# Performance work log

Measured on AMD Instinct MI355X. Metric: run time of the kernel, lower is better.

The kernel has to match this reference:

```python
import jax, jax.numpy as jnp
import numpy as np
from jax import lax

C, NORI, NROT, K, PAD = 256, 8, 2, 3, 1
B, H, W = 16, 64, 64
EPS = 1e-5


def setup_inputs() -> dict:
    key = jax.random.key(0)
    k1, k2, k3 = jax.random.split(key, 3)
    x = jax.random.normal(k1, (B, C, H, W), dtype=jnp.float32)
    # rotate_arf() output: [nRot*C, nOri*C, K, K]
    weight_all = jax.random.normal(k2, (NROT * C, NORI * C, K, K), dtype=jnp.float32) * 0.02
    bias_all = jax.random.normal(k3, (NROT * C,), dtype=jnp.float32) * 0.02
    alpha = jnp.float32(1.0)
    gamma = jnp.ones((C,), dtype=jnp.float32)
    beta = jnp.zeros((C,), dtype=jnp.float32)
    return {"x": x, "weight_all": weight_all, "bias_all": bias_all,
            "alpha": alpha, "gamma": gamma, "beta": beta}


def _forward(x, weight_all, bias_all, alpha, gamma, beta):
    # Loop of nOri*nRot convs over the same x with different weight blocks,
    # all accumulated into one [B,C,H,W] tensor == single conv with summed blocks
    # (conv is linear in the weights): fused form of the original loop.
    W_eff = weight_all.reshape(NROT, C, NORI, C, K, K).sum(axis=(0, 2))  # [C, C, K, K]
    b_eff = bias_all.reshape(NROT, C).sum(axis=0) * NORI                 # [C]
    d_sum = lax.conv_general_dilated(
        x, W_eff, window_strides=(1, 1), padding=[(PAD, PAD), (PAD, PAD)],
        dimension_numbers=("NCHW", "OIHW", "NCHW"))
    d_sum = d_sum + b_eff[None, :, None, None]
    d_mean = d_sum / float(NORI * NROT)
    out = x + alpha * d_mean
    # BatchNorm2d, training mode: biased batch stats over (B, H, W)
    mean = out.mean(axis=(0, 2, 3))
    var = ((out - mean[None, :, None, None]) ** 2).mean(axis=(0, 2, 3))
    inv = lax.rsqrt(var + EPS)
    y = (out - mean[None, :, None, None]) * (gamma * inv)[None, :, None, None] \
        + beta[None, :, None, None]
    return y


def reference(x, weight_all, bias_all, alpha, gamma, beta):
    return _forward(x, weight_all, bias_all, alpha, gamma, beta)
```

## Files before the change

kernel.cpp:

```cpp
#include <hip/hip_runtime.h>
#include <stdint.h>

typedef __attribute__((__ext_vector_type__(8))) __bf16 bf16x8;
typedef __attribute__((__ext_vector_type__(4))) float  f32x4;

#define XT_OFF    0ul
#define WT_OFF    33554432ul
#define BEFF_OFF  34734080ul
#define ZERO_OFF  34737152ul
#define STATS_OFF 34737408ul

__device__ inline void gload_lds16(const void* g, void* l) {
  __builtin_amdgcn_global_load_lds((const __attribute__((address_space(1))) void*)g,
                                   (__attribute__((address_space(3))) void*)l,
                                   16, 0, 0);
}

__global__ void k_wred(const float* __restrict__ w, const float* __restrict__ bias,
                       const float* __restrict__ alpha_p, __bf16* __restrict__ Wt,
                       float* __restrict__ beff, float* __restrict__ zerob,
                       float* __restrict__ statsG) {
  const int co = blockIdx.x;
  const int ci = threadIdx.x;
  float a[9];
#pragma unroll
  for (int t = 0; t < 9; ++t) a[t] = 0.f;
#pragma unroll
  for (int r = 0; r < 2; ++r)
#pragma unroll
    for (int o = 0; o < 8; ++o) {
      const float* p = w + ((size_t)(r * 256 + co) * 2048 + (size_t)(o * 256 + ci)) * 9;
#pragma unroll
      for (int t = 0; t < 9; ++t) a[t] += p[t];
    }
  const float sc = alpha_p[0] * 0.0625f;
  const int s = ci >> 6, cis = ci & 63;
#pragma unroll
  for (int t = 0; t < 9; ++t)
    Wt[(size_t)(t * 4 + s) * 16384 + co * 64 + cis] = (__bf16)(a[t] * sc);
  if (ci == 0) beff[co] = (bias[co] + bias[256 + co]) * 8.0f * sc;
  if (blockIdx.x == 0) {
    statsG[ci] = 0.f; statsG[256 + ci] = 0.f;
    if (ci < 64) zerob[ci] = 0.f;
  }
}

__global__ void k_xpose(const float* __restrict__ x, __bf16* __restrict__ xT) {
  __shared__ __bf16 lds[64 * 258];
  int bh = blockIdx.x;
  int b = bh >> 6, h = bh & 63;
  int t = threadIdx.x;
  int w = t & 63, cg = t >> 6;
  const float* xb = x + ((size_t)b * 16384 + h) * 64;
#pragma unroll 4
  for (int cb = 0; cb < 256; cb += 4) {
    int ci = cb + cg;
    lds[w * 258 + ci] = (__bf16)xb[(size_t)ci * 4096 + w];
  }
  __syncthreads();
  const uint32_t* l32 = (const uint32_t*)lds;
  uint32_t* o32 = (uint32_t*)(xT + ((size_t)b * 64 + h) * 64 * 256);
  int c2 = t & 127, wg = t >> 7;
  for (int w0 = 0; w0 < 64; w0 += 2) {
    int ww = w0 + wg;
    o32[ww * 128 + c2] = l32[ww * 129 + c2];
  }
}

#define A_BYTES 51200
#define B_BYTES 32768

#define MFMA16(RH, AV, BV)                                                      \
  _Pragma("unroll")                                                             \
  for (int j = 0; j < 4; ++j) {                                                 \
    _Pragma("unroll")                                                           \
    for (int q = 0; q < 4; ++q)                                                 \
      acc[(RH) * 4 + q][j] =                                                    \
        __builtin_amdgcn_mfma_f32_16x16x32_bf16(AV[q], BV[j],                   \
                                                acc[(RH) * 4 + q][j], 0, 0, 0); \
  }

__global__ __launch_bounds__(512) void k_conv(
    const float* __restrict__ x, const __bf16* __restrict__ xT,
    const __bf16* __restrict__ Wt, const float* __restrict__ beff,
    const __bf16* __restrict__ zerob, float* __restrict__ out,
    float* __restrict__ statsG)
{
  __shared__ __align__(16) char lds[A_BYTES + 3 * B_BYTES];
  const int bb   = blockIdx.x >> 4;
  const int ho0  = (blockIdx.x & 15) << 2;
  const int tid  = threadIdx.x;
  const int lane = tid & 63;
  const int wid  = tid >> 6;
  const int wr   = wid >> 2;
  const int wc   = wid & 3;
  const int l15  = lane & 15;

  f32x4 acc[8][4];
#pragma unroll
  for (int i = 0; i < 8; ++i)
#pragma unroll
    for (int j = 0; j < 4; ++j)
#pragma unroll
      for (int r = 0; r < 4; ++r) acc[i][j][r] = 0.f;

  const char* zb = (const char*)zerob;

  const int co0 = (wc << 6) + l15;
  const int bb0 = (((co0 << 7) + ((lane >> 4) << 4)) ^ ((co0 & 7) << 4));
  const int bb1 = (((co0 << 7) + ((lane >> 4) << 4) + 64) ^ ((co0 & 7) << 4));
  const int bl = lane >> 3;
  const int bsrcLane = (bl << 7) + (((lane & 7) ^ (bl & 7)) << 4);

  auto stageA = [&](int s) {
    const int ci0 = s << 6;
    for (int t = wid; t < 50; t += 8) {
      const int ch = (t << 3) + (lane >> 3);
      const int r  = ch / 66;
      const int c  = ch - r * 66;
      const int ir = ho0 - 1 + r;
      const int ic = c - 1;
      const int k  = (lane & 7) ^ (ch & 7);
      const char* src;
      if (ch < 396 && ir >= 0 && ir < 64 && ic >= 0 && ic < 64)
        src = (const char*)(xT + ((((size_t)bb << 6) + ir) * 64 + ic) * 256 + ci0 + (k << 3));
      else
        src = zb + (k << 4);
      gload_lds16(src, lds + (t << 10));
    }
  };

  auto stageB = [&](int ph, int bi) {
    char* buf = lds + A_BYTES + bi * B_BYTES;
    const int s2 = ph / 9, tp = ph - s2 * 9;
    const char* wsrc = (const char*)Wt + ((size_t)(tp * 4 + s2) << 15) + bsrcLane;
#pragma unroll
    for (int it = 0; it < 4; ++it) {
      const int t = wid + (it << 3);
      gload_lds16(wsrc + (t << 10), buf + (t << 10));
    }
  };

  stageA(0);
  stageB(0, 0);
  stageB(1, 1);
  asm volatile("s_waitcnt vmcnt(4)" ::: "memory");
  __builtin_amdgcn_s_barrier();

  int s = 0, tap = 0, bcur = 0;
  for (int p = 0; p < 36; ++p) {
    if (p > 0) {
      if (p == 35) asm volatile("s_waitcnt vmcnt(0)" ::: "memory");
      else         asm volatile("s_waitcnt vmcnt(4)" ::: "memory");
      __builtin_amdgcn_s_barrier();
    }
    const bool bnd = (tap == 0) && (p > 0);
    if (bnd) stageA(s);
    if (p + 2 < 36) {
      int bnx = bcur + 2; if (bnx >= 3) bnx -= 3;
      stageB(p + 2, bnx);
    }
    if (bnd) asm volatile("s_waitcnt vmcnt(4)" ::: "memory");

    const int dh = (tap >= 6) ? 2 : (tap >= 3 ? 1 : 0);
    const int dw = tap - dh * 3;
    const char* Bb = lds + A_BYTES + bcur * B_BYTES;
    const int pr0  = ((wr << 1) + dh) * 66 + l15 + dw;
    const int pr1  = pr0 + 66;
    const int cib  = (lane >> 4) << 4;
    const int ab00 = (((pr0 << 7) + cib) ^ ((pr0 & 7) << 4));
    const int ab01 = (((pr1 << 7) + cib) ^ ((pr1 & 7) << 4));
    const int ab10 = (((pr0 << 7) + cib + 64) ^ ((pr0 & 7) << 4));
    const int ab11 = (((pr1 << 7) + cib + 64) ^ ((pr1 & 7) << 4));

    bf16x8 bv0[4], bv1[4], a0[4], a1[4], a2[4], a3[4];
#pragma unroll
    for (int j = 0; j < 4; ++j) bv0[j] = *(const bf16x8*)(Bb + bb0 + (j << 11));
#pragma unroll
    for (int j = 0; j < 4; ++j) bv1[j] = *(const bf16x8*)(Bb + bb1 + (j << 11));
#pragma unroll
    for (int q = 0; q < 4; ++q) a0[q] = *(const bf16x8*)(lds + ab00 + (q << 11));
#pragma unroll
    for (int q = 0; q < 4; ++q) a1[q] = *(const bf16x8*)(lds + ab01 + (q << 11));

    __builtin_amdgcn_s_setprio(1);
    MFMA16(0, a0, bv0);
    __builtin_amdgcn_s_setprio(0);
#pragma unroll
    for (int q = 0; q < 4; ++q) a2[q] = *(const bf16x8*)(lds + ab10 + (q << 11));
    __builtin_amdgcn_s_setprio(1);
    MFMA16(1, a1, bv0);
    __builtin_amdgcn_s_setprio(0);
#pragma unroll
    for (int q = 0; q < 4; ++q) a3[q] = *(const bf16x8*)(lds + ab11 + (q << 11));
    __builtin_amdgcn_s_setprio(1);
    MFMA16(0, a2, bv1);
    MFMA16(1, a3, bv1);
    __builtin_amdgcn_s_setprio(0);

    if (++tap == 9) { tap = 0; ++s; }
    if (++bcur == 3) bcur = 0;
  }

  __syncthreads();
  float* sw    = (float*)lds + wid * 2064;
  float* lstat = (float*)(lds + 131072);
  if (tid < 512) lstat[tid] = 0.f;
  __syncthreads();

  const int cl = lane & 15, ch4 = (lane >> 4) << 2;
  const int cc2 = lane >> 2, q2 = lane & 3;
#pragma unroll
  for (int j = 0; j < 4; ++j) {
#pragma unroll
    for (int i = 0; i < 8; ++i)
#pragma unroll
      for (int r = 0; r < 4; ++r)
        sw[cl * 129 + (i << 4) + ch4 + r] = acc[i][j][r];
    for (int cc = 0; cc < 16; ++cc) {
      const int co = (wc << 6) + (j << 4) + cc;
      const float be = beff[co];
#pragma unroll
      for (int half = 0; half < 2; ++half) {
        const float conv = sw[cc * 129 + (half << 6) + lane];
        const int ho = ho0 + (wr << 1) + half;
        const size_t oi = ((((size_t)bb << 8) + (size_t)co) << 12) + (ho << 6) + lane;
        const float v = x[oi] + conv + be;
        out[oi] = v;
        sw[cc * 129 + (half << 6) + lane] = v;
      }
    }
    float r1 = 0.f, r2 = 0.f;
#pragma unroll
    for (int k = 0; k < 32; ++k) {
      const float vv = sw[cc2 * 129 + (q2 << 5) + k];
      r1 += vv; r2 += vv * vv;
    }
    r1 += __shfl_xor(r1, 1); r2 += __shfl_xor(r2, 1);
    r1 += __shfl_xor(r1, 2); r2 += __shfl_xor(r2, 2);
    if (q2 == 0) {
      const int co = (wc << 6) + (j << 4) + cc2;
      atomicAdd(&lstat[co], r1);
      atomicAdd(&lstat[256 + co], r2);
    }
    __syncthreads();
  }
  if (tid < 512) atomicAdd(&statsG[tid], lstat[tid]);
}

__global__ void k_apply(float* __restrict__ out, const float* __restrict__ statsG,
                        const float* __restrict__ gamma, const float* __restrict__ beta) {
  size_t i = (size_t)blockIdx.x * 256 + threadIdx.x;
  int co = (int)((i >> 10) & 255);
  const float mean = statsG[co] * (1.f / 65536.f);
  const float var  = statsG[256 + co] * (1.f / 65536.f) - mean * mean;
  const float inv  = rsqrtf(var + 1e-5f);
  const float sc   = gamma[co] * inv;
  const float sh   = beta[co] - mean * sc;
  float4* p = (float4*)out;
  float4 v = p[i];
  v.x = v.x * sc + sh; v.y = v.y * sc + sh; v.z = v.z * sc + sh; v.w = v.w * sc + sh;
  p[i] = v;
}

extern "C" void kernel_launch(void* const* d_in, const int* in_sizes, int n_in,
                              void* d_out, int out_size, void* d_ws, size_t ws_size,
                              hipStream_t stream) {
  const float* x     = (const float*)d_in[0];
  const float* wall  = (const float*)d_in[1];
  const float* bias  = (const float*)d_in[2];
  const float* alpha = (const float*)d_in[3];
  const float* gamma = (const float*)d_in[4];
  const float* beta  = (const float*)d_in[5];
  float* out = (float*)d_out;

  char* ws = (char*)d_ws;
  __bf16* xT     = (__bf16*)(ws + XT_OFF);
  __bf16* Wt     = (__bf16*)(ws + WT_OFF);
  float*  beff   = (float*)(ws + BEFF_OFF);
  float*  zerob  = (float*)(ws + ZERO_OFF);
  float*  statsG = (float*)(ws + STATS_OFF);

  k_wred<<<256, 256, 0, stream>>>(wall, bias, alpha, Wt, beff, zerob, statsG);
  k_xpose<<<1024, 256, 0, stream>>>(x, xT);
  k_conv<<<256, 512, 0, stream>>>(x, xT, Wt, beff, (const __bf16*)zerob, out, statsG);
  k_apply<<<16384, 256, 0, stream>>>(out, statsG, gamma, beta);
}
```

Measured before the change: 129.7 us.

## Split main loop into barrier-fenced sub-phases interleaving B prefetch with MFMA

Restructures the conv main loop into four sub-phases per tap. Each sub-phase loads its LDS fragments, issues half of the next weight prefetch, then runs its MFMA block between barriers at raised priority, so waves stay in lockstep and memory issue overlaps compute. The A-tile restage moves to the end of each 9-tap channel group and waits fully with vmcnt(0). This adds eight barriers per iteration and a full drain at each channel-block boundary. The weight buffer is three deep and refilled two taps ahead, so overwrite safety depends on these new barriers.

```diff
diff --git a/kernel.cpp b/kernel.cpp
--- a/kernel.cpp
+++ b/kernel.cpp
@@ -79,6 +79,12 @@
         __builtin_amdgcn_mfma_f32_16x16x32_bf16(AV[q], BV[j],                   \
                                                 acc[(RH) * 4 + q][j], 0, 0, 0); \
   }
+
+#define SUBPHASE_OPEN()  __builtin_amdgcn_s_barrier();                          \
+                         asm volatile("s_waitcnt lgkmcnt(0)" ::: "memory");     \
+                         __builtin_amdgcn_s_setprio(1)
+#define SUBPHASE_CLOSE() __builtin_amdgcn_s_setprio(0);                         \
+                         __builtin_amdgcn_s_barrier()
 
 __global__ __launch_bounds__(512) void k_conv(
     const float* __restrict__ x, const __bf16* __restrict__ xT,
@@ -130,38 +136,25 @@
     }
   };
 
-  auto stageB = [&](int ph, int bi) {
+  auto stageB2 = [&](int ph, int bi, int half) {
     char* buf = lds + A_BYTES + bi * B_BYTES;
     const int s2 = ph / 9, tp = ph - s2 * 9;
     const char* wsrc = (const char*)Wt + ((size_t)(tp * 4 + s2) << 15) + bsrcLane;
 #pragma unroll
-    for (int it = 0; it < 4; ++it) {
-      const int t = wid + (it << 3);
+    for (int it = 0; it < 2; ++it) {
+      const int t = wid + (((half << 1) + it) << 3);
       gload_lds16(wsrc + (t << 10), buf + (t << 10));
     }
   };
 
   stageA(0);
-  stageB(0, 0);
-  stageB(1, 1);
+  stageB2(0, 0, 0); stageB2(0, 0, 1);
+  stageB2(1, 1, 0); stageB2(1, 1, 1);
   asm volatile("s_waitcnt vmcnt(4)" ::: "memory");
   __builtin_amdgcn_s_barrier();
 
   int s = 0, tap = 0, bcur = 0;
   for (int p = 0; p < 36; ++p) {
-    if (p > 0) {
-      if (p == 35) asm volatile("s_waitcnt vmcnt(0)" ::: "memory");
-      else         asm volatile("s_waitcnt vmcnt(4)" ::: "memory");
-      __builtin_amdgcn_s_barrier();
-    }
-    const bool bnd = (tap == 0) && (p > 0);
-    if (bnd) stageA(s);
-    if (p + 2 < 36) {
-      int bnx = bcur + 2; if (bnx >= 3) bnx -= 3;
-      stageB(p + 2, bnx);
-    }
-    if (bnd) asm volatile("s_waitcnt vmcnt(4)" ::: "memory");
-
     const int dh = (tap >= 6) ? 2 : (tap >= 3 ? 1 : 0);
     const int dw = tap - dh * 3;
     const char* Bb = lds + A_BYTES + bcur * B_BYTES;
@@ -172,33 +165,51 @@
     const int ab01 = (((pr1 << 7) + cib) ^ ((pr1 & 7) << 4));
     const int ab10 = (((pr0 << 7) + cib + 64) ^ ((pr0 & 7) << 4));
     const int ab11 = (((pr1 << 7) + cib + 64) ^ ((pr1 & 7) << 4));
+    const bool hv  = (p + 2 < 36);
+    int bnx = bcur + 2; if (bnx >= 3) bnx -= 3;
 
     bf16x8 bv0[4], bv1[4], a0[4], a1[4], a2[4], a3[4];
+
 #pragma unroll
     for (int j = 0; j < 4; ++j) bv0[j] = *(const bf16x8*)(Bb + bb0 + (j << 11));
 #pragma unroll
+    for (int q = 0; q < 4; ++q) a0[q] = *(const bf16x8*)(lds + ab00 + (q << 11));
+    if (hv) stageB2(p + 2, bnx, 0);
+    SUBPHASE_OPEN();
+    MFMA16(0, a0, bv0);
+    SUBPHASE_CLOSE();
+
+#pragma unroll
+    for (int q = 0; q < 4; ++q) a1[q] = *(const bf16x8*)(lds + ab01 + (q << 11));
+    if (hv) stageB2(p + 2, bnx, 1);
+    SUBPHASE_OPEN();
+    MFMA16(1, a1, bv0);
+    SUBPHASE_CLOSE();
+
+#pragma unroll
     for (int j = 0; j < 4; ++j) bv1[j] = *(const bf16x8*)(Bb + bb1 + (j << 11));
 #pragma unroll
-    for (int q = 0; q < 4; ++q) a0[q] = *(const bf16x8*)(lds + ab00 + (q << 11));
-#pragma unroll
-    for (int q = 0; q < 4; ++q) a1[q] = *(const bf16x8*)(lds + ab01 + (q << 11));
-
-    __builtin_amdgcn_s_setprio(1);
-    MFMA16(0, a0, bv0);
-    __builtin_amdgcn_s_setprio(0);
-#pragma unroll
     for (int q = 0; q < 4; ++q) a2[q] = *(const bf16x8*)(lds + ab10 + (q << 11));
-    __builtin_amdgcn_s_setprio(1);
-    MFMA16(1, a1, bv0);
-    __builtin_amdgcn_s_setprio(0);
+    SUBPHASE_OPEN();
+    MFMA16(0, a2, bv1);
+    SUBPHASE_CLOSE();
+
 #pragma unroll
     for (int q = 0; q < 4; ++q) a3[q] = *(const bf16x8*)(lds + ab11 + (q << 11));
-    __builtin_amdgcn_s_setprio(1);
-    MFMA16(0, a2, bv1);
+    if (hv) asm volatile("s_waitcnt vmcnt(4)" ::: "memory");
+    else    asm volatile("s_waitcnt vmcnt(0)" ::: "memory");
+    SUBPHASE_OPEN();
     MFMA16(1, a3, bv1);
-    __builtin_amdgcn_s_setprio(0);
-
-    if (++tap == 9) { tap = 0; ++s; }
+    SUBPHASE_CLOSE();
+
+    if (++tap == 9) {
+      tap = 0; ++s;
+      if (s < 4) {
+        stageA(s);
+        asm volatile("s_waitcnt vmcnt(0)" ::: "memory");
+        __builtin_amdgcn_s_barrier();
+      }
+    }
     if (++bcur == 3) bcur = 0;
   }
 
```

Result: no change. 131.0 us (+1.0%).

## Load conv weights directly into registers and double-buffer input slabs in LDS

Applied to the files above, without the earlier changes.

Weight fragments are no longer staged through a triple-buffered LDS ring. Each wave now loads them straight from global memory into ping-pong register arrays, one phase ahead. The input slab is double-buffered in LDS, so block barriers are needed only at slab boundaries instead of every phase, and the per-iteration barrier in the epilogue is dropped. Launch bounds now request two blocks per CU, which caps registers even though the accumulators already use 128 values per lane and could spill. The LDS footprint still likely allows only one block per CU.

```diff
diff --git a/kernel.cpp b/kernel.cpp
--- a/kernel.cpp
+++ b/kernel.cpp
@@ -68,25 +68,24 @@
 }
 
 #define A_BYTES 51200
-#define B_BYTES 32768
-
-#define MFMA16(RH, AV, BV)                                                      \
+
+#define MFMAq(RH, AV, B, KO)                                                    \
   _Pragma("unroll")                                                             \
   for (int j = 0; j < 4; ++j) {                                                 \
     _Pragma("unroll")                                                           \
     for (int q = 0; q < 4; ++q)                                                 \
       acc[(RH) * 4 + q][j] =                                                    \
-        __builtin_amdgcn_mfma_f32_16x16x32_bf16(AV[q], BV[j],                   \
+        __builtin_amdgcn_mfma_f32_16x16x32_bf16(AV[q], (B)[(KO) + j],           \
                                                 acc[(RH) * 4 + q][j], 0, 0, 0); \
   }
 
-__global__ __launch_bounds__(512) void k_conv(
+__global__ __launch_bounds__(512, 2) void k_conv(
     const float* __restrict__ x, const __bf16* __restrict__ xT,
     const __bf16* __restrict__ Wt, const float* __restrict__ beff,
     const __bf16* __restrict__ zerob, float* __restrict__ out,
     float* __restrict__ statsG)
 {
-  __shared__ __align__(16) char lds[A_BYTES + 3 * B_BYTES];
+  __shared__ __align__(16) char lds[2 * A_BYTES + 2048];
   const int bb   = blockIdx.x >> 4;
   const int ho0  = (blockIdx.x & 15) << 2;
   const int tid  = threadIdx.x;
@@ -106,14 +105,21 @@
 
   const char* zb = (const char*)zerob;
 
-  const int co0 = (wc << 6) + l15;
-  const int bb0 = (((co0 << 7) + ((lane >> 4) << 4)) ^ ((co0 & 7) << 4));
-  const int bb1 = (((co0 << 7) + ((lane >> 4) << 4) + 64) ^ ((co0 & 7) << 4));
-  const int bl = lane >> 3;
-  const int bsrcLane = (bl << 7) + (((lane & 7) ^ (bl & 7)) << 4);
+  const int bregBase = (((wc << 6) + l15) << 7) + ((lane >> 4) << 4);
+
+  auto loadB = [&](int ph, bf16x8* dst) {
+    const int s2 = ph / 9, tp = ph - s2 * 9;
+    const char* wn = (const char*)Wt + ((size_t)(tp * 4 + s2) << 15) + bregBase;
+#pragma unroll
+    for (int kk = 0; kk < 2; ++kk)
+#pragma unroll
+      for (int j = 0; j < 4; ++j)
+        dst[(kk << 2) + j] = *(const bf16x8*)(wn + (j << 11) + (kk << 6));
+  };
 
   auto stageA = [&](int s) {
     const int ci0 = s << 6;
+    char* buf = lds + (s & 1) * A_BYTES;
     for (int t = wid; t < 50; t += 8) {
       const int ch = (t << 3) + (lane >> 3);
       const int r  = ch / 66;
@@ -126,45 +132,19 @@
         src = (const char*)(xT + ((((size_t)bb << 6) + ir) * 64 + ic) * 256 + ci0 + (k << 3));
       else
         src = zb + (k << 4);
-      gload_lds16(src, lds + (t << 10));
+      gload_lds16(src, buf + (t << 10));
     }
   };
 
-  auto stageB = [&](int ph, int bi) {
-    char* buf = lds + A_BYTES + bi * B_BYTES;
-    const int s2 = ph / 9, tp = ph - s2 * 9;
-    const char* wsrc = (const char*)Wt + ((size_t)(tp * 4 + s2) << 15) + bsrcLane;
-#pragma unroll
-    for (int it = 0; it < 4; ++it) {
-      const int t = wid + (it << 3);
-      gload_lds16(wsrc + (t << 10), buf + (t << 10));
-    }
-  };
-
-  stageA(0);
-  stageB(0, 0);
-  stageB(1, 1);
-  asm volatile("s_waitcnt vmcnt(4)" ::: "memory");
-  __builtin_amdgcn_s_barrier();
-
-  int s = 0, tap = 0, bcur = 0;
-  for (int p = 0; p < 36; ++p) {
-    if (p > 0) {
-      if (p == 35) asm volatile("s_waitcnt vmcnt(0)" ::: "memory");
-      else         asm volatile("s_waitcnt vmcnt(4)" ::: "memory");
-      __builtin_amdgcn_s_barrier();
-    }
-    const bool bnd = (tap == 0) && (p > 0);
-    if (bnd) stageA(s);
-    if (p + 2 < 36) {
-      int bnx = bcur + 2; if (bnx >= 3) bnx -= 3;
-      stageB(p + 2, bnx);
-    }
-    if (bnd) asm volatile("s_waitcnt vmcnt(4)" ::: "memory");
-
+  bf16x8 bA[8], bB[8];
+
+  auto phase = [&](int p, bf16x8* cur, bf16x8* nxt) {
+    const int s2 = p / 9, tap = p - s2 * 9;
+    if (p + 1 < 36) loadB(p + 1, nxt);
+    if (tap == 0 && s2 < 3) stageA(s2 + 1);
+    const char* slab = lds + (s2 & 1) * A_BYTES;
     const int dh = (tap >= 6) ? 2 : (tap >= 3 ? 1 : 0);
     const int dw = tap - dh * 3;
-    const char* Bb = lds + A_BYTES + bcur * B_BYTES;
     const int pr0  = ((wr << 1) + dh) * 66 + l15 + dw;
     const int pr1  = pr0 + 66;
     const int cib  = (lane >> 4) << 4;
@@ -173,38 +153,47 @@
     const int ab10 = (((pr0 << 7) + cib + 64) ^ ((pr0 & 7) << 4));
     const int ab11 = (((pr1 << 7) + cib + 64) ^ ((pr1 & 7) << 4));
 
-    bf16x8 bv0[4], bv1[4], a0[4], a1[4], a2[4], a3[4];
-#pragma unroll
-    for (int j = 0; j < 4; ++j) bv0[j] = *(const bf16x8*)(Bb + bb0 + (j << 11));
-#pragma unroll
-    for (int j = 0; j < 4; ++j) bv1[j] = *(const bf16x8*)(Bb + bb1 + (j << 11));
-#pragma unroll
-    for (int q = 0; q < 4; ++q) a0[q] = *(const bf16x8*)(lds + ab00 + (q << 11));
-#pragma unroll
-    for (int q = 0; q < 4; ++q) a1[q] = *(const bf16x8*)(lds + ab01 + (q << 11));
-
-    __builtin_amdgcn_s_setprio(1);
-    MFMA16(0, a0, bv0);
-    __builtin_amdgcn_s_setprio(0);
-#pragma unroll
-    for (int q = 0; q < 4; ++q) a2[q] = *(const bf16x8*)(lds + ab10 + (q << 11));
-    __builtin_amdgcn_s_setprio(1);
-    MFMA16(1, a1, bv0);
-    __builtin_amdgcn_s_setprio(0);
-#pragma unroll
-    for (int q = 0; q < 4; ++q) a3[q] = *(const bf16x8*)(lds + ab11 + (q << 11));
-    __builtin_amdgcn_s_setprio(1);
-    MFMA16(0, a2, bv1);
-    MFMA16(1, a3, bv1);
-    __builtin_amdgcn_s_setprio(0);
-
-    if (++tap == 9) { tap = 0; ++s; }
-    if (++bcur == 3) bcur = 0;
+    bf16x8 a0[4], a1[4], a2[4], a3[4];
+#pragma unroll
+    for (int q = 0; q < 4; ++q) a0[q] = *(const bf16x8*)(slab + ab00 + (q << 11));
+    __builtin_amdgcn_s_setprio(1);
+    MFMAq(0, a0, cur, 0);
+    __builtin_amdgcn_s_setprio(0);
+#pragma unroll
+    for (int q = 0; q < 4; ++q) a1[q] = *(const bf16x8*)(slab + ab01 + (q << 11));
+    __builtin_amdgcn_s_setprio(1);
+    MFMAq(1, a1, cur, 0);
+    __builtin_amdgcn_s_setprio(0);
+#pragma unroll
+    for (int q = 0; q < 4; ++q) a2[q] = *(const bf16x8*)(slab + ab10 + (q << 11));
+    __builtin_amdgcn_s_setprio(1);
+    MFMAq(0, a2, cur, 4);
+    __builtin_amdgcn_s_setprio(0);
+#pragma unroll
+    for (int q = 0; q < 4; ++q) a3[q] = *(const bf16x8*)(slab + ab11 + (q << 11));
+    __builtin_amdgcn_s_setprio(1);
+    MFMAq(1, a3, cur, 4);
+    __builtin_amdgcn_s_setprio(0);
+
+    if (tap == 8 && s2 < 3) {
+      asm volatile("s_waitcnt vmcnt(8)" ::: "memory");
+      __builtin_amdgcn_s_barrier();
+    }
+  };
+
+  stageA(0);
+  loadB(0, bA);
+  asm volatile("s_waitcnt vmcnt(8)" ::: "memory");
+  __builtin_amdgcn_s_barrier();
+
+  for (int pp = 0; pp < 18; ++pp) {
+    phase(2 * pp,     bA, bB);
+    phase(2 * pp + 1, bB, bA);
   }
 
   __syncthreads();
   float* sw    = (float*)lds + wid * 2064;
-  float* lstat = (float*)(lds + 131072);
+  float* lstat = (float*)(lds + 2 * A_BYTES);
   if (tid < 512) lstat[tid] = 0.f;
   __syncthreads();
 
@@ -243,8 +232,8 @@
       atomicAdd(&lstat[co], r1);
       atomicAdd(&lstat[256 + co], r2);
     }
-    __syncthreads();
-  }
+  }
+  __syncthreads();
   if (tid < 512) atomicAdd(&statsG[tid], lstat[tid]);
 }
 
```

Result: slower. 170.9 us (+31.8%).
